# Performance work log

Hardware: AMD Instinct MI355X
Metric: run time of the kernel (lower is better)

Reference implementation:

```python
import jax, jax.numpy as jnp
import numpy as np

N_NODES = 10000
N_EDGES = 100000
D = 248        # algebra_dim (E8)
H = 512        # hidden_dim of update MLP
NNZ = 2480     # nonzero structure-constant triples (~10 per basis element)
LN_EPS = 1e-5


def setup_inputs() -> dict:
    key = jax.random.key(0)
    ks = jax.random.split(key, 12)
    features = jax.random.normal(ks[0], (N_NODES, D), dtype=jnp.float32)
    edge_index = jax.random.randint(ks[1], (2, N_EDGES), 0, N_NODES, dtype=jnp.int32)
    # Linear weights (torch convention: y = x @ W.T + b)
    W_msg = jax.random.normal(ks[2], (D, D), dtype=jnp.float32) / np.sqrt(D)
    W1 = jax.random.normal(ks[3], (H, D), dtype=jnp.float32) / np.sqrt(D)
    b1 = jnp.zeros((H,), dtype=jnp.float32)
    W2 = jax.random.normal(ks[4], (D, H), dtype=jnp.float32) / np.sqrt(H)
    b2 = jnp.zeros((D,), dtype=jnp.float32)
    gamma = jnp.ones((D,), dtype=jnp.float32)
    beta = jnp.zeros((D,), dtype=jnp.float32)
    # Sparse Lie-bracket structure constants: bracket(x, y)[K_t] += C_t * x[I_t] * y[J_t]
    I = jax.random.randint(ks[5], (NNZ,), 0, D, dtype=jnp.int32)
    J = jax.random.randint(ks[6], (NNZ,), 0, D, dtype=jnp.int32)
    K = jax.random.randint(ks[7], (NNZ,), 0, D, dtype=jnp.int32)
    C = jax.random.normal(ks[8], (NNZ,), dtype=jnp.float32) * 0.1
    return {"features": features, "edge_index": edge_index, "W_msg": W_msg,
            "W1": W1, "b1": b1, "W2": W2, "b2": b2,
            "gamma": gamma, "beta": beta, "I": I, "J": J, "K": K, "C": C}


def _layer_norm(x, gamma, beta):
    mu = jnp.mean(x, axis=-1, keepdims=True)
    xc = x - mu
    var = jnp.mean(xc * xc, axis=-1, keepdims=True)
    return xc * jax.lax.rsqrt(var + LN_EPS) * gamma + beta


def reference(features, edge_index, W_msg, W1, b1, W2, b2, gamma, beta, I, J, K, C):
    src, tgt = edge_index[0], edge_index[1]
    src_proj = features[src] @ W_msg.T           # (E, D) edge gather + linear
    tgt_feats = features[tgt]                    # (E, D)
    # sparse Lie bracket: out[e, K_t] += C_t * src_proj[e, I_t] * tgt_feats[e, J_t]
    prod = src_proj[:, I] * tgt_feats[:, J] * C  # (E, NNZ)
    messages = jnp.zeros((src.shape[0], D), features.dtype).at[:, K].add(prod)
    # scatter-add messages onto target nodes
    agg = jax.ops.segment_sum(messages, tgt, num_segments=N_NODES)  # (N, D)
    # residual MLP update + LayerNorm
    h = jax.nn.silu(agg @ W1.T + b1) @ W2.T + b2
    return _layer_norm(features + h, gamma, beta)
```

## Files before the change

kernel.cpp:

```cpp
#include <hip/hip_runtime.h>
#include <hip/hip_fp16.h>

#define N_NODES 10000
#define N_EDGES 100000
#define D 248
#define DP 256
#define HDIM 512
#define NNZ 2480
#define LN_EPS 1e-5f
#define PAD_ROWS 128
#define NTHR 256
#define CAP 32
#define PBLK 157

typedef __attribute__((ext_vector_type(8))) _Float16 f16x8_t;
typedef __attribute__((ext_vector_type(4))) float f32x4_t;

__device__ __forceinline__ unsigned short f2h(float f) {
  return __builtin_bit_cast(unsigned short, __float2half(f));
}
__device__ __forceinline__ unsigned packh2(float a, float b) {
  return __builtin_bit_cast(unsigned, __floats2half2_rn(a, b));
}
__device__ __forceinline__ void gload_lds16(const unsigned short* gp,
                                            unsigned short* lds_base) {
  __builtin_amdgcn_global_load_lds(
      (const __attribute__((address_space(1))) void*)gp,
      (__attribute__((address_space(3))) void*)lds_base, 16, 0, 0);
}

__device__ __forceinline__ void cast_row_dev(const float* src, unsigned short* dst,
                                             int r, int sr, int sc, int dc) {
  for (int c = threadIdx.x; c < dc; c += NTHR) {
    float v = (r < sr && c < sc) ? src[(size_t)r * sc + c] : 0.f;
    dst[(size_t)r * dc + c] = f2h(v);
  }
}

#define G1U 628
#define UF_END (G1U + 1250)
#define UW1_END (UF_END + 512)
#define UW2_END (UW1_END + 256)
#define UCSR_END (UW2_END + 1)
#define HIST_U ((N_EDGES + 255) / 256)
#define FRONT_BLOCKS (UCSR_END + HIST_U)

__global__ __launch_bounds__(NTHR) void front_kernel(
    const float* __restrict__ features, const float* __restrict__ W_msg,
    const float* __restrict__ W1, const float* __restrict__ W2,
    const int* __restrict__ ei,
    unsigned short* __restrict__ featH, unsigned short* __restrict__ W1H,
    unsigned short* __restrict__ W2H, unsigned short* __restrict__ S2H,
    const int* __restrict__ Iv, const int* __restrict__ Jv,
    const int* __restrict__ Kv, const float* __restrict__ Cv,
    int* __restrict__ rsK, int2* __restrict__ trip,
    int* __restrict__ deg, int* __restrict__ ovfc,
    int* __restrict__ esrc, int2* __restrict__ ovf) {
  __shared__ union {
    struct { unsigned short As[4096]; unsigned short Bs[4096]; } g;
    struct { int cnt[D]; int off[D]; } csr;
  } sm;
  const int u = blockIdx.x;
  const int tid = threadIdx.x;

  if (u < G1U) {
    const int wave = tid >> 6;
    const int lane = tid & 63;
    const int wm = wave >> 1;
    const int wn = wave & 1;
    const int ml = lane & 15;
    const int q = lane >> 4;
    const int sr = tid >> 3;
    const int scg = tid & 7;
    const int n0 = (u & 3) << 6;
    const int m0 = (u >> 2) << 6;

    f32x4_t acc[2][2];
#pragma unroll
    for (int i = 0; i < 2; i++)
#pragma unroll
      for (int j = 0; j < 2; j++) acc[i][j] = (f32x4_t)0.f;

    for (int kb = 0; kb < 4; kb++) {
      const int g8 = kb * 8 + scg;
#pragma unroll
      for (int r2 = 0; r2 < 2; r2++) {
        const int row = r2 * 32 + sr;
        uint4 o = make_uint4(0u, 0u, 0u, 0u);
        if (m0 + row < N_NODES && g8 < 31) {
          const float* p = features + (size_t)(m0 + row) * D + g8 * 8;
          float4 v0 = *(const float4*)p;
          float4 v1 = *(const float4*)(p + 4);
          o.x = packh2(v0.x, v0.y); o.y = packh2(v0.z, v0.w);
          o.z = packh2(v1.x, v1.y); o.w = packh2(v1.z, v1.w);
        }
        *(uint4*)(sm.g.As + row * 64 + (scg ^ (row & 7)) * 8) = o;
      }
#pragma unroll
      for (int r2 = 0; r2 < 2; r2++) {
        const int row = r2 * 32 + sr;
        uint4 o = make_uint4(0u, 0u, 0u, 0u);
        if (n0 + row < D && g8 < 31) {
          const float* p = W_msg + (size_t)(n0 + row) * D + g8 * 8;
          float4 v0 = *(const float4*)p;
          float4 v1 = *(const float4*)(p + 4);
          o.x = packh2(v0.x, v0.y); o.y = packh2(v0.z, v0.w);
          o.z = packh2(v1.x, v1.y); o.w = packh2(v1.z, v1.w);
        }
        *(uint4*)(sm.g.Bs + row * 64 + (scg ^ (row & 7)) * 8) = o;
      }
      __syncthreads();
#pragma unroll
      for (int kk = 0; kk < 2; kk++) {
        f16x8_t a[2], b[2];
#pragma unroll
        for (int im = 0; im < 2; im++) {
          int row = wm * 32 + im * 16 + ml;
          a[im] = *(const f16x8_t*)(sm.g.As + row * 64 + ((kk * 4 + q) ^ (row & 7)) * 8);
        }
#pragma unroll
        for (int jn = 0; jn < 2; jn++) {
          int row = wn * 32 + jn * 16 + ml;
          b[jn] = *(const f16x8_t*)(sm.g.Bs + row * 64 + ((kk * 4 + q) ^ (row & 7)) * 8);
        }
#pragma unroll
        for (int im = 0; im < 2; im++)
#pragma unroll
          for (int jn = 0; jn < 2; jn++)
            acc[im][jn] = __builtin_amdgcn_mfma_f32_16x16x32_f16(
                a[im], b[jn], acc[im][jn], 0, 0, 0);
      }
      __syncthreads();
    }
#pragma unroll
    for (int im = 0; im < 2; im++) {
#pragma unroll
      for (int jn = 0; jn < 2; jn++) {
        int gn = n0 + wn * 32 + jn * 16 + ml;
#pragma unroll
        for (int reg = 0; reg < 4; reg++) {
          int gm = m0 + wm * 32 + im * 16 + q * 4 + reg;
          if (gm < N_NODES)
            S2H[(size_t)gm * DP + gn] = f2h(acc[im][jn][reg]);
        }
      }
    }
  } else if (u < UF_END) {
    const int r = (u - G1U) * 8 + (tid >> 5);
    const int c = tid & 31;
    uint4 o = make_uint4(0u, 0u, 0u, 0u);
    if (c < 31) {
      const float* src = features + (size_t)r * D + c * 8;
      float4 v0 = *(const float4*)(src);
      float4 v1 = *(const float4*)(src + 4);
      o.x = packh2(v0.x, v0.y);
      o.y = packh2(v0.z, v0.w);
      o.z = packh2(v1.x, v1.y);
      o.w = packh2(v1.z, v1.w);
    }
    *(uint4*)(featH + (size_t)r * DP + c * 8) = o;
  } else if (u < UW1_END) {
    cast_row_dev(W1, W1H, u - UF_END, HDIM, D, DP);
  } else if (u < UW2_END) {
    cast_row_dev(W2, W2H, u - UW1_END, D, HDIM, HDIM);
  } else if (u < UCSR_END) {
    for (int k = tid; k < D; k += NTHR) sm.csr.cnt[k] = 0;
    __syncthreads();
    for (int t = tid; t < NNZ; t += NTHR) atomicAdd(&sm.csr.cnt[Kv[t]], 1);
    __syncthreads();
    if (tid == 0) {
      int run = 0;
      for (int k = 0; k < D; k++) { sm.csr.off[k] = run; rsK[k] = run; run += sm.csr.cnt[k]; }
      rsK[D] = run;
    }
    __syncthreads();
    for (int t = tid; t < NNZ; t += NTHR) {
      int pos = atomicAdd(&sm.csr.off[Kv[t]], 1);
      trip[pos] = make_int2((Jv[t] << 16) | Iv[t], __float_as_int(Cv[t]));
    }
  } else {
    int e = (u - UCSR_END) * 256 + tid;
    if (e < N_EDGES) {
      int src = ei[e];
      int tgt = ei[N_EDGES + e];
      int r = atomicAdd(&deg[tgt], 1);
      if (r < CAP) {
        esrc[tgt * CAP + r] = src;
      } else {
        int o = atomicAdd(ovfc, 1);
        ovf[o] = make_int2(tgt, src);
      }
    }
  }
}

template <int EPI>
__global__ __launch_bounds__(NTHR) void gemm_kernel(
    const unsigned short* __restrict__ A, const unsigned short* __restrict__ B,
    const float* __restrict__ bias, void* __restrict__ Cout,
    int M, int ncl2, int K, int lda, int ldb, int ldc) {
  __shared__ unsigned short As[64 * 64];
  __shared__ unsigned short Bs[64 * 64];
  const int tid = threadIdx.x;
  const int wave = tid >> 6;
  const int lane = tid & 63;
  const int wm = wave >> 1;
  const int wn = wave & 1;
  const int ml = lane & 15;
  const int q = lane >> 4;
  const int srow = lane >> 3;
  const int sg = lane & 7;
  const int sgs = sg ^ srow;
  const int ncol = 1 << ncl2;
  const int tile = blockIdx.x;
  const int n0 = (tile & (ncol - 1)) << 6;
  const int m0 = (tile >> ncl2) << 6;

  f32x4_t acc[2][2];
#pragma unroll
  for (int i = 0; i < 2; i++)
#pragma unroll
    for (int j = 0; j < 2; j++) acc[i][j] = (f32x4_t)0.f;

  for (int k0 = 0; k0 < K; k0 += 64) {
#pragma unroll
    for (int i = 0; i < 2; i++) {
      int t = wave * 2 + i;
      gload_lds16(A + (size_t)(m0 + t * 8 + srow) * lda + k0 + sgs * 8, As + t * 512);
    }
#pragma unroll
    for (int i = 0; i < 2; i++) {
      int t = wave * 2 + i;
      gload_lds16(B + (size_t)(n0 + t * 8 + srow) * ldb + k0 + sgs * 8, Bs + t * 512);
    }
    __syncthreads();
#pragma unroll
    for (int kk = 0; kk < 2; kk++) {
      f16x8_t a[2], b[2];
#pragma unroll
      for (int im = 0; im < 2; im++) {
        int row = wm * 32 + im * 16 + ml;
        int c8 = (kk * 4 + q) ^ (row & 7);
        a[im] = *(const f16x8_t*)(As + row * 64 + c8 * 8);
      }
#pragma unroll
      for (int jn = 0; jn < 2; jn++) {
        int row = wn * 32 + jn * 16 + ml;
        int c8 = (kk * 4 + q) ^ (row & 7);
        b[jn] = *(const f16x8_t*)(Bs + row * 64 + c8 * 8);
      }
#pragma unroll
      for (int im = 0; im < 2; im++)
#pragma unroll
        for (int jn = 0; jn < 2; jn++)
          acc[im][jn] = __builtin_amdgcn_mfma_f32_16x16x32_f16(
              a[im], b[jn], acc[im][jn], 0, 0, 0);
    }
    __syncthreads();
  }

#pragma unroll
  for (int im = 0; im < 2; im++) {
#pragma unroll
    for (int jn = 0; jn < 2; jn++) {
      int gn = n0 + wn * 32 + jn * 16 + ml;
#pragma unroll
      for (int reg = 0; reg < 4; reg++) {
        int gm = m0 + wm * 32 + im * 16 + q * 4 + reg;
        if (gm >= M) continue;
        float v = acc[im][jn][reg];
        if (EPI == 1) {
          v += bias[gn];
          v = v / (1.f + __expf(-v));
          ((unsigned short*)Cout)[(size_t)gm * ldc + gn] = f2h(v);
        } else {
          v += (gn < D) ? bias[gn] : 0.f;
          ((float*)Cout)[(size_t)gm * ldc + gn] = v;
        }
      }
    }
  }
}

__global__ __launch_bounds__(NTHR) void gather_bracket(
    const unsigned short* __restrict__ S2H, const unsigned short* __restrict__ FH,
    const int* __restrict__ deg, const int* __restrict__ esrc,
    const int* __restrict__ ovfc, const int2* __restrict__ ovf,
    const int* __restrict__ rsK, const int2* __restrict__ trip,
    unsigned short* __restrict__ agg) {
  __shared__ unsigned sSg[8][DP / 2];
  __shared__ unsigned sS2[4][DP];
  __shared__ unsigned sF2[4][DP];
  const int tid = threadIdx.x;
  const int lane = tid & 63;
  const int half = lane >> 5;
  const int c = lane & 31;
  const int node8 = tid >> 5;
  const int n = blockIdx.x * 8 + node8;

  {
    const int dg = deg[n];
    const int dc = (dg < CAP) ? dg : CAP;
    int eid = (c < dc) ? esrc[n * CAP + c] : 0;

    __half2 a0 = __floats2half2_rn(0.f, 0.f), a1 = a0, a2 = a0, a3 = a0;
    __half2 b0 = a0, b1 = a0, b2 = a0, b3 = a0;
    const unsigned short* Sc = S2H + (size_t)c * 8;
    int j = 0;
    for (; j + 2 <= dc; j += 2) {
      int s0 = __shfl(eid, half * 32 + j);
      int s1 = __shfl(eid, half * 32 + j + 1);
      uint4 u0 = *(const uint4*)(Sc + (size_t)s0 * DP);
      uint4 u1 = *(const uint4*)(Sc + (size_t)s1 * DP);
      a0 = __hadd2(a0, __builtin_bit_cast(__half2, u0.x));
      a1 = __hadd2(a1, __builtin_bit_cast(__half2, u0.y));
      a2 = __hadd2(a2, __builtin_bit_cast(__half2, u0.z));
      a3 = __hadd2(a3, __builtin_bit_cast(__half2, u0.w));
      b0 = __hadd2(b0, __builtin_bit_cast(__half2, u1.x));
      b1 = __hadd2(b1, __builtin_bit_cast(__half2, u1.y));
      b2 = __hadd2(b2, __builtin_bit_cast(__half2, u1.z));
      b3 = __hadd2(b3, __builtin_bit_cast(__half2, u1.w));
    }
    if (j < dc) {
      int s = __shfl(eid, half * 32 + j);
      uint4 u0 = *(const uint4*)(Sc + (size_t)s * DP);
      a0 = __hadd2(a0, __builtin_bit_cast(__half2, u0.x));
      a1 = __hadd2(a1, __builtin_bit_cast(__half2, u0.y));
      a2 = __hadd2(a2, __builtin_bit_cast(__half2, u0.z));
      a3 = __hadd2(a3, __builtin_bit_cast(__half2, u0.w));
    }
    if (dg > CAP) {
      int novf = *ovfc;
      for (int o = 0; o < novf; o++) {
        int2 e = ovf[o];
        if (e.x == n) {
          uint4 u0 = *(const uint4*)(Sc + (size_t)e.y * DP);
          a0 = __hadd2(a0, __builtin_bit_cast(__half2, u0.x));
          a1 = __hadd2(a1, __builtin_bit_cast(__half2, u0.y));
          a2 = __hadd2(a2, __builtin_bit_cast(__half2, u0.z));
          a3 = __hadd2(a3, __builtin_bit_cast(__half2, u0.w));
        }
      }
    }
    unsigned* d = &sSg[node8][c * 4];
    d[0] = __builtin_bit_cast(unsigned, __hadd2(a0, b0));
    d[1] = __builtin_bit_cast(unsigned, __hadd2(a1, b1));
    d[2] = __builtin_bit_cast(unsigned, __hadd2(a2, b2));
    d[3] = __builtin_bit_cast(unsigned, __hadd2(a3, b3));
  }
  __syncthreads();

  const int wv = tid >> 6;
  const int n0 = blockIdx.x * 8 + wv * 2;
  const int n1 = n0 + 1;
  {
#pragma unroll
    for (int j = 0; j < 4; j++) {
      int k = lane * 4 + j;
      unsigned w0 = sSg[wv * 2][lane * 2 + (j >> 1)];
      unsigned w1 = sSg[wv * 2 + 1][lane * 2 + (j >> 1)];
      unsigned h0 = (j & 1) ? (w0 >> 16) : (w0 & 0xFFFF);
      unsigned h1 = (j & 1) ? (w1 >> 16) : (w1 & 0xFFFF);
      sS2[wv][k] = h0 | (h1 << 16);
    }
    ushort4 u0 = *(const ushort4*)(FH + (size_t)n0 * DP + lane * 4);
    ushort4 u1 = *(const ushort4*)(FH + (size_t)n1 * DP + lane * 4);
    unsigned* d = &sF2[wv][lane * 4];
    d[0] = (unsigned)u0.x | ((unsigned)u1.x << 16);
    d[1] = (unsigned)u0.y | ((unsigned)u1.y << 16);
    d[2] = (unsigned)u0.z | ((unsigned)u1.z << 16);
    d[3] = (unsigned)u0.w | ((unsigned)u1.w << 16);
  }
  __syncthreads();

  const unsigned* S2 = sS2[wv];
  const unsigned* F2 = sF2[wv];
#pragma unroll
  for (int kk = 0; kk < 4; kk++) {
    const int k = lane + kk * 64;
    float a0 = 0.f, a1 = 0.f, b0 = 0.f, b1 = 0.f;
    if (k < D) {
      const int tb = rsK[k], te = rsK[k + 1];
      int t = tb;
      for (; t + 2 <= te; t += 2) {
        int2 t0 = trip[t], t1 = trip[t + 1];
        __half2 p0 = __hmul2(__builtin_bit_cast(__half2, S2[t0.x & 0xFFFF]),
                             __builtin_bit_cast(__half2, F2[t0.x >> 16]));
        __half2 p1 = __hmul2(__builtin_bit_cast(__half2, S2[t1.x & 0xFFFF]),
                             __builtin_bit_cast(__half2, F2[t1.x >> 16]));
        float2 q0 = __half22float2(p0);
        float2 q1 = __half22float2(p1);
        const float c0 = __int_as_float(t0.y), c1 = __int_as_float(t1.y);
        a0 += c0 * q0.x; a1 += c0 * q0.y;
        b0 += c1 * q1.x; b1 += c1 * q1.y;
      }
      if (t < te) {
        int2 t0 = trip[t];
        __half2 p0 = __hmul2(__builtin_bit_cast(__half2, S2[t0.x & 0xFFFF]),
                             __builtin_bit_cast(__half2, F2[t0.x >> 16]));
        float2 q0 = __half22float2(p0);
        const float c0 = __int_as_float(t0.y);
        a0 += c0 * q0.x; a1 += c0 * q0.y;
      }
    }
    agg[(size_t)n0 * DP + k] = f2h(a0 + b0);
    agg[(size_t)n1 * DP + k] = f2h(a1 + b1);
  }
}

__global__ __launch_bounds__(NTHR) void ln_kernel(
    const float* __restrict__ x0, const float* __restrict__ h2,
    const float* __restrict__ gamma, const float* __restrict__ beta,
    float* __restrict__ out) {
  const int tid = threadIdx.x;
  const int wv = tid >> 6;
  const int lane = tid & 63;
  const int n = blockIdx.x * 4 + wv;

  float4 x = make_float4(0.f, 0.f, 0.f, 0.f);
  if (lane < 62) {
    float4 f = *(const float4*)(x0 + (size_t)n * D + lane * 4);
    float4 h = *(const float4*)(h2 + (size_t)n * DP + lane * 4);
    x = make_float4(f.x + h.x, f.y + h.y, f.z + h.z, f.w + h.w);
  }
  float s = x.x + x.y + x.z + x.w;
#pragma unroll
  for (int o = 32; o > 0; o >>= 1) s += __shfl_xor(s, o);
  const float mu = s * (1.f / (float)D);
  float4 xc = make_float4(x.x - mu, x.y - mu, x.z - mu, x.w - mu);
  float v = 0.f;
  if (lane < 62) v = xc.x * xc.x + xc.y * xc.y + xc.z * xc.z + xc.w * xc.w;
#pragma unroll
  for (int o = 32; o > 0; o >>= 1) v += __shfl_xor(v, o);
  const float rstd = rsqrtf(v * (1.f / (float)D) + LN_EPS);
  if (lane < 62) {
    float4 g = *(const float4*)(gamma + lane * 4);
    float4 b = *(const float4*)(beta + lane * 4);
    float4 o;
    o.x = xc.x * rstd * g.x + b.x;
    o.y = xc.y * rstd * g.y + b.y;
    o.z = xc.z * rstd * g.z + b.z;
    o.w = xc.w * rstd * g.w + b.w;
    *(float4*)(out + (size_t)n * D + lane * 4) = o;
  }
}

extern "C" void kernel_launch(void* const* d_in, const int* in_sizes, int n_in,
                              void* d_out, int out_size, void* d_ws, size_t ws_size,
                              hipStream_t stream) {
  const float* features = (const float*)d_in[0];
  const int*   ei       = (const int*)d_in[1];
  const float* W_msg    = (const float*)d_in[2];
  const float* W1       = (const float*)d_in[3];
  const float* b1       = (const float*)d_in[4];
  const float* W2       = (const float*)d_in[5];
  const float* b2       = (const float*)d_in[6];
  const float* gamma    = (const float*)d_in[7];
  const float* beta     = (const float*)d_in[8];
  const int*   Iv       = (const int*)d_in[9];
  const int*   Jv       = (const int*)d_in[10];
  const int*   Kv       = (const int*)d_in[11];
  const float* Cv       = (const float*)d_in[12];
  float* out = (float*)d_out;

  char* cur = (char*)d_ws;
  auto alloc = [&](size_t bytes) {
    char* p = cur;
    cur += (bytes + 255) & ~(size_t)255;
    return p;
  };
  const size_t NP = (size_t)N_NODES + PAD_ROWS;
  unsigned short* featH = (unsigned short*)alloc(NP * DP * 2);
  unsigned short* W1H   = (unsigned short*)alloc((size_t)HDIM * DP * 2);
  unsigned short* W2H   = (unsigned short*)alloc((size_t)DP * HDIM * 2);
  unsigned short* S2H   = (unsigned short*)alloc(NP * DP * 2);
  unsigned short* aggH  = (unsigned short*)alloc(NP * DP * 2);
  unsigned short* H1H   = (unsigned short*)alloc(NP * HDIM * 2);
  float*          H2    = (float*)alloc((size_t)N_NODES * DP * 4);
  int*  rsK  = (int*)alloc((D + 1) * 4);
  int2* trip = (int2*)alloc(NNZ * 8);
  int*  deg  = (int*)alloc((N_NODES + 64) * 4);
  int*  ovfc = deg + N_NODES;
  int*  esrc = (int*)alloc((size_t)N_NODES * CAP * 4);
  int2* ovf  = (int2*)alloc((size_t)N_EDGES * 8);

  dim3 blk(NTHR);

  hipMemsetAsync(deg, 0, (size_t)(N_NODES + 1) * 4, stream);
  front_kernel<<<FRONT_BLOCKS, blk, 0, stream>>>(
      features, W_msg, W1, W2, ei, featH, W1H, W2H, S2H,
      Iv, Jv, Kv, Cv, rsK, trip, deg, ovfc, esrc, ovf);
  gather_bracket<<<N_NODES / 8, blk, 0, stream>>>(
      S2H, featH, deg, esrc, ovfc, ovf, rsK, trip, aggH);
  gemm_kernel<1><<<PBLK * 8, blk, 0, stream>>>(
      aggH, W1H, b1, H1H, N_NODES, 3, DP, DP, DP, HDIM);
  gemm_kernel<2><<<PBLK * 4, blk, 0, stream>>>(
      H1H, W2H, b2, H2, N_NODES, 2, HDIM, HDIM, HDIM, DP);
  ln_kernel<<<N_NODES / 4, blk, 0, stream>>>(features, H2, gamma, beta, out);
}
```

Before: 162.6 us.

## Fuse second MLP GEMM with residual add and LayerNorm epilogue

Result: slower. 181.3 us (+11.5%).

```diff
diff --git a/kernel.cpp b/kernel.cpp
--- a/kernel.cpp
+++ b/kernel.cpp
@@ -194,10 +194,9 @@
   }
 }
 
-template <int EPI>
-__global__ __launch_bounds__(NTHR) void gemm_kernel(
+__global__ __launch_bounds__(NTHR) void gemm2_kernel(
     const unsigned short* __restrict__ A, const unsigned short* __restrict__ B,
-    const float* __restrict__ bias, void* __restrict__ Cout,
+    const float* __restrict__ bias, unsigned short* __restrict__ Cout,
     int M, int ncl2, int K, int lda, int ldb, int ldc) {
   __shared__ unsigned short As[64 * 64];
   __shared__ unsigned short Bs[64 * 64];
@@ -240,14 +239,12 @@
 #pragma unroll
       for (int im = 0; im < 2; im++) {
         int row = wm * 32 + im * 16 + ml;
-        int c8 = (kk * 4 + q) ^ (row & 7);
-        a[im] = *(const f16x8_t*)(As + row * 64 + c8 * 8);
+        a[im] = *(const f16x8_t*)(As + row * 64 + ((kk * 4 + q) ^ (row & 7)) * 8);
       }
 #pragma unroll
       for (int jn = 0; jn < 2; jn++) {
         int row = wn * 32 + jn * 16 + ml;
-        int c8 = (kk * 4 + q) ^ (row & 7);
-        b[jn] = *(const f16x8_t*)(Bs + row * 64 + c8 * 8);
+        b[jn] = *(const f16x8_t*)(Bs + row * 64 + ((kk * 4 + q) ^ (row & 7)) * 8);
       }
 #pragma unroll
       for (int im = 0; im < 2; im++)
@@ -268,15 +265,9 @@
       for (int reg = 0; reg < 4; reg++) {
         int gm = m0 + wm * 32 + im * 16 + q * 4 + reg;
         if (gm >= M) continue;
-        float v = acc[im][jn][reg];
-        if (EPI == 1) {
-          v += bias[gn];
-          v = v / (1.f + __expf(-v));
-          ((unsigned short*)Cout)[(size_t)gm * ldc + gn] = f2h(v);
-        } else {
-          v += (gn < D) ? bias[gn] : 0.f;
-          ((float*)Cout)[(size_t)gm * ldc + gn] = v;
-        }
+        float v = acc[im][jn][reg] + bias[gn];
+        v = v / (1.f + __expf(-v));
+        Cout[(size_t)gm * ldc + gn] = f2h(v);
       }
     }
   }
@@ -408,40 +399,145 @@
   }
 }
 
-__global__ __launch_bounds__(NTHR) void ln_kernel(
-    const float* __restrict__ x0, const float* __restrict__ h2,
+__global__ __launch_bounds__(NTHR) void gemm3_ln_kernel(
+    const unsigned short* __restrict__ H1H,
+    const unsigned short* __restrict__ W2H,
+    const float* __restrict__ b2,
+    const float* __restrict__ features,
     const float* __restrict__ gamma, const float* __restrict__ beta,
     float* __restrict__ out) {
+  __shared__ unsigned short As[64 * 64];
+  __shared__ unsigned short Bs[256 * 64];
+  __shared__ float lnp[4][64];
+
   const int tid = threadIdx.x;
-  const int wv = tid >> 6;
+  const int wave = tid >> 6;
+  const int wv = wave;
   const int lane = tid & 63;
-  const int n = blockIdx.x * 4 + wv;
-
-  float4 x = make_float4(0.f, 0.f, 0.f, 0.f);
-  if (lane < 62) {
-    float4 f = *(const float4*)(x0 + (size_t)n * D + lane * 4);
-    float4 h = *(const float4*)(h2 + (size_t)n * DP + lane * 4);
-    x = make_float4(f.x + h.x, f.y + h.y, f.z + h.z, f.w + h.w);
-  }
-  float s = x.x + x.y + x.z + x.w;
-#pragma unroll
-  for (int o = 32; o > 0; o >>= 1) s += __shfl_xor(s, o);
-  const float mu = s * (1.f / (float)D);
-  float4 xc = make_float4(x.x - mu, x.y - mu, x.z - mu, x.w - mu);
-  float v = 0.f;
-  if (lane < 62) v = xc.x * xc.x + xc.y * xc.y + xc.z * xc.z + xc.w * xc.w;
-#pragma unroll
-  for (int o = 32; o > 0; o >>= 1) v += __shfl_xor(v, o);
-  const float rstd = rsqrtf(v * (1.f / (float)D) + LN_EPS);
-  if (lane < 62) {
-    float4 g = *(const float4*)(gamma + lane * 4);
-    float4 b = *(const float4*)(beta + lane * 4);
-    float4 o;
-    o.x = xc.x * rstd * g.x + b.x;
-    o.y = xc.y * rstd * g.y + b.y;
-    o.z = xc.z * rstd * g.z + b.z;
-    o.w = xc.w * rstd * g.w + b.w;
-    *(float4*)(out + (size_t)n * D + lane * 4) = o;
+  const int ml = lane & 15;
+  const int q = lane >> 4;
+  const int srow = lane >> 3;
+  const int sg = lane & 7;
+  const int sgs = sg ^ srow;
+  const int m0 = blockIdx.x * 64;
+
+  f32x4_t h2[4][4];
+#pragma unroll
+  for (int im = 0; im < 4; im++)
+#pragma unroll
+    for (int jn = 0; jn < 4; jn++) h2[im][jn] = (f32x4_t)0.f;
+
+  for (int k0 = 0; k0 < HDIM; k0 += 64) {
+#pragma unroll
+    for (int i = 0; i < 2; i++) {
+      int t = wave * 2 + i;
+      gload_lds16(H1H + (size_t)(m0 + t * 8 + srow) * HDIM + k0 + sgs * 8,
+                  As + t * 512);
+    }
+#pragma unroll
+    for (int i = 0; i < 8; i++) {
+      int t = wave * 8 + i;
+      gload_lds16(W2H + (size_t)(t * 8 + srow) * HDIM + k0 + sgs * 8,
+                  Bs + t * 512);
+    }
+    __syncthreads();
+#pragma unroll
+    for (int kk = 0; kk < 2; kk++) {
+      f16x8_t a[4], b[4];
+#pragma unroll
+      for (int im = 0; im < 4; im++) {
+        int row = im * 16 + ml;
+        a[im] = *(const f16x8_t*)(As + row * 64 + ((kk * 4 + q) ^ (row & 7)) * 8);
+      }
+#pragma unroll
+      for (int jn = 0; jn < 4; jn++) {
+        int row = wv * 64 + jn * 16 + ml;
+        b[jn] = *(const f16x8_t*)(Bs + row * 64 + ((kk * 4 + q) ^ (row & 7)) * 8);
+      }
+#pragma unroll
+      for (int im = 0; im < 4; im++)
+#pragma unroll
+        for (int jn = 0; jn < 4; jn++)
+          h2[im][jn] = __builtin_amdgcn_mfma_f32_16x16x32_f16(
+              a[im], b[jn], h2[im][jn], 0, 0, 0);
+    }
+    __syncthreads();
+  }
+
+  float mu[4][4], rstd[4][4];
+#pragma unroll
+  for (int im = 0; im < 4; im++) {
+#pragma unroll
+    for (int reg = 0; reg < 4; reg++) {
+      const int gm = m0 + im * 16 + q * 4 + reg;
+      float s = 0.f;
+#pragma unroll
+      for (int jn = 0; jn < 4; jn++) {
+        const int col = wv * 64 + jn * 16 + ml;
+        float x = 0.f;
+        if (col < D && gm < N_NODES)
+          x = h2[im][jn][reg] + b2[col] + features[(size_t)gm * D + col];
+        h2[im][jn][reg] = x;
+        s += x;
+      }
+#pragma unroll
+      for (int o = 8; o > 0; o >>= 1) s += __shfl_xor(s, o);
+      if (ml == 0) lnp[wv][im * 16 + q * 4 + reg] = s;
+    }
+  }
+  __syncthreads();
+#pragma unroll
+  for (int im = 0; im < 4; im++)
+#pragma unroll
+    for (int reg = 0; reg < 4; reg++) {
+      int r = im * 16 + q * 4 + reg;
+      mu[im][reg] = (lnp[0][r] + lnp[1][r] + lnp[2][r] + lnp[3][r]) * (1.f / (float)D);
+    }
+  __syncthreads();
+#pragma unroll
+  for (int im = 0; im < 4; im++) {
+#pragma unroll
+    for (int reg = 0; reg < 4; reg++) {
+      const int gm = m0 + im * 16 + q * 4 + reg;
+      float ss = 0.f;
+#pragma unroll
+      for (int jn = 0; jn < 4; jn++) {
+        const int col = wv * 64 + jn * 16 + ml;
+        if (col < D && gm < N_NODES) {
+          float xc = h2[im][jn][reg] - mu[im][reg];
+          ss += xc * xc;
+        }
+      }
+#pragma unroll
+      for (int o = 8; o > 0; o >>= 1) ss += __shfl_xor(ss, o);
+      if (ml == 0) lnp[wv][im * 16 + q * 4 + reg] = ss;
+    }
+  }
+  __syncthreads();
+#pragma unroll
+  for (int im = 0; im < 4; im++)
+#pragma unroll
+    for (int reg = 0; reg < 4; reg++) {
+      int r = im * 16 + q * 4 + reg;
+      float var = (lnp[0][r] + lnp[1][r] + lnp[2][r] + lnp[3][r]) * (1.f / (float)D);
+      rstd[im][reg] = rsqrtf(var + LN_EPS);
+    }
+#pragma unroll
+  for (int im = 0; im < 4; im++) {
+#pragma unroll
+    for (int jn = 0; jn < 4; jn++) {
+      const int col = wv * 64 + jn * 16 + ml;
+      if (col >= D) continue;
+      const float g = gamma[col];
+      const float bt = beta[col];
+#pragma unroll
+      for (int reg = 0; reg < 4; reg++) {
+        const int gm = m0 + im * 16 + q * 4 + reg;
+        if (gm < N_NODES)
+          out[(size_t)gm * D + col] =
+              (h2[im][jn][reg] - mu[im][reg]) * rstd[im][reg] * g + bt;
+      }
+    }
   }
 }
 
@@ -476,7 +572,6 @@
   unsigned short* S2H   = (unsigned short*)alloc(NP * DP * 2);
   unsigned short* aggH  = (unsigned short*)alloc(NP * DP * 2);
   unsigned short* H1H   = (unsigned short*)alloc(NP * HDIM * 2);
-  float*          H2    = (float*)alloc((size_t)N_NODES * DP * 4);
   int*  rsK  = (int*)alloc((D + 1) * 4);
   int2* trip = (int2*)alloc(NNZ * 8);
   int*  deg  = (int*)alloc((N_NODES + 64) * 4);
@@ -492,9 +587,8 @@
       Iv, Jv, Kv, Cv, rsK, trip, deg, ovfc, esrc, ovf);
   gather_bracket<<<N_NODES / 8, blk, 0, stream>>>(
       S2H, featH, deg, esrc, ovfc, ovf, rsK, trip, aggH);
-  gemm_kernel<1><<<PBLK * 8, blk, 0, stream>>>(
+  gemm2_kernel<<<PBLK * 8, blk, 0, stream>>>(
       aggH, W1H, b1, H1H, N_NODES, 3, DP, DP, DP, HDIM);
-  gemm_kernel<2><<<PBLK * 4, blk, 0, stream>>>(
-      H1H, W2H, b2, H2, N_NODES, 2, HDIM, HDIM, HDIM, DP);
-  ln_kernel<<<N_NODES / 4, blk, 0, stream>>>(features, H2, gamma, beta, out);
-}
+  gemm3_ln_kernel<<<PBLK, blk, 0, stream>>>(
+      H1H, W2H, b2, features, gamma, beta, out);
+}
```
